# Optimization experiments

Measured on AMD Instinct MI355X. Metric: run time of the kernel, lower is better.

The kernel has to match this reference:

```python
import jax, jax.numpy as jnp
import numpy as np

B, N, F = 32, 64, 128   # batch, nodes, input features (F == hidden_dim)
E = N * (N - 1)         # fully-connected directed edges = 4032
H, D = 4, 64            # heads, out_dim per head
ALPHA = 0.2             # leaky relu slope


def setup_inputs() -> dict:
    key = jax.random.key(0)
    ks = jax.random.split(key, 16)
    v_self = jax.random.normal(ks[0], (B, N, F), dtype=jnp.float32)
    # fully-connected one-hot sender/receiver matrices [E, N], broadcast to [B, E, N]
    pairs = np.array([(i, j) for i in range(N) for j in range(N) if i != j])
    send = np.zeros((E, N), np.float32); send[np.arange(E), pairs[:, 0]] = 1.0
    rec = np.zeros((E, N), np.float32); rec[np.arange(E), pairs[:, 1]] = 1.0
    rel_send = jnp.broadcast_to(jnp.asarray(send), (B, E, N))
    rel_rec = jnp.broadcast_to(jnp.asarray(rec), (B, E, N))
    s = 0.05
    return {
        "v_self": v_self,
        "rel_rec": rel_rec,
        "rel_send": rel_send,
        "W_proj": jax.random.normal(ks[1], (H * D, F), dtype=jnp.float32) * s,
        "a_fwd": jax.random.normal(ks[2], (H, D), dtype=jnp.float32) * s,
        "a_bwd": jax.random.normal(ks[3], (H, D), dtype=jnp.float32) * s,
        "We1": jax.random.normal(ks[4], (D, 2 * D), dtype=jnp.float32) * s,
        "be1": jnp.zeros((D,), jnp.float32),
        "We2": jax.random.normal(ks[5], (D, D), dtype=jnp.float32) * s,
        "be2": jnp.zeros((D,), jnp.float32),
        "Wv1": jax.random.normal(ks[6], (F, D), dtype=jnp.float32) * s,
        "bv1": jnp.zeros((F,), jnp.float32),
        "Wv2": jax.random.normal(ks[7], (F, F), dtype=jnp.float32) * s,
        "bv2": jnp.zeros((F,), jnp.float32),
        "Wv3": jax.random.normal(ks[8], (D, F), dtype=jnp.float32) * s,
        "bv3": jnp.zeros((D,), jnp.float32),
    }


def _leaky(x):
    return jnp.where(x >= 0, x, ALPHA * x)


def reference(v_self, rel_rec, rel_send, W_proj, a_fwd, a_bwd,
              We1, be1, We2, be2, Wv1, bv1, Wv2, bv2, Wv3, bv3):
    # project: [B,N,F] -> [B,N,H,D]
    v_proj = (v_self @ W_proj.T).reshape(B, N, H, D)
    # gather to edges via one-hot adjacency (v_src==h_src, v_tgt==h_tgt in original)
    h_src = jnp.einsum('ben,bnhd->behd', rel_send, v_proj)
    h_tgt = jnp.einsum('ben,bnhd->behd', rel_rec, v_proj)
    attn_ij = _leaky(jnp.einsum('behd,hd->beh', h_src, a_fwd)) / 500.0
    attn_ji = _leaky(jnp.einsum('behd,hd->beh', h_tgt, a_bwd)) / 500.0
    attn_max = jnp.maximum(attn_ij, attn_ji)
    # NOTE: original applies exp twice (exp of exp); reproduced faithfully
    e_ij = jnp.exp(jnp.exp(attn_ij - attn_max))
    e_ji = jnp.exp(jnp.exp(attn_ji - attn_max))
    alpha_sum = e_ij + e_ji
    alpha_ij = e_ij / alpha_sum   # [B,E,H]
    alpha_ji = e_ji / alpha_sum
    edge_input = jnp.concatenate(
        [alpha_ij[..., None] * h_src, alpha_ji[..., None] * h_tgt], axis=-1)  # [B,E,H,2D]
    # f_CG_e: Linear(2D->D), ReLU, Linear(D->D) on last dim
    e_cg = jax.nn.relu(edge_input @ We1.T + be1) @ We2.T + be2
    edge_weighted = e_cg * alpha_ij[..., None]                               # [B,E,H,D]
    # scatter back to nodes
    v_social = jnp.einsum('behd,ben->bnhd', edge_weighted, rel_rec)          # [B,N,H,D]
    # f_CG_v: Linear(D->F), ReLU, Linear(F->F), ReLU, Linear(F->D)
    x = jax.nn.relu(v_social @ Wv1.T + bv1)
    x = jax.nn.relu(x @ Wv2.T + bv2)
    x = x @ Wv3.T + bv3
    v_out = x.reshape(B, N, H * D)  # concat_heads=True
    return (v_out, alpha_ij)
```

## Files before the change

kernel.cpp:

```cpp
#include <hip/hip_runtime.h>

#define B_ 32
#define N_ 64
#define F_ 128
#define E_ 4032
#define H_ 4
#define D_ 64

typedef __bf16 bf16x8 __attribute__((ext_vector_type(8)));
typedef __bf16 bf16x4 __attribute__((ext_vector_type(4)));
typedef float  f32x4  __attribute__((ext_vector_type(4)));


__global__ __launch_bounds__(256) void k_proj(
    const float* __restrict__ v_self, const float* __restrict__ W_proj,
    const float* __restrict__ We1,
    const float* __restrict__ a_fwd, const float* __restrict__ a_bwd,
    float* __restrict__ s_fwd, float* __restrict__ s_bwd,
    __bf16* __restrict__ u_src, __bf16* __restrict__ u_tgt)
{
    const int t = threadIdx.x;
    const int w = t >> 6, l = t & 63;
    const int q = l >> 4, lr = l & 15;
    const int node0 = blockIdx.x * 8;

    __shared__ __bf16 Av[16 * 136];
    __shared__ __bf16 P_lds[8 * 288];

    {
        int row = t >> 5, c0 = (t & 31) * 4;
        float4 v = *(const float4*)(v_self + (size_t)(node0 + row) * 128 + c0);
        bf16x4 bv; bv[0]=(__bf16)v.x; bv[1]=(__bf16)v.y; bv[2]=(__bf16)v.z; bv[3]=(__bf16)v.w;
        *(bf16x4*)&Av[row * 136 + c0] = bv;
        bf16x4 z = {};
        *(bf16x4*)&Av[(row + 8) * 136 + c0] = z;
    }
    __syncthreads();

    f32x4 acc[4] = {};
#pragma unroll
    for (int ks = 0; ks < 4; ++ks) {
        bf16x8 a = *(const bf16x8*)&Av[lr * 136 + ks * 32 + q * 8];
#pragma unroll
        for (int ct = 0; ct < 4; ++ct) {
            const float4* wr = (const float4*)(W_proj + (size_t)(w * 64 + ct * 16 + lr) * 128 + ks * 32 + q * 8);
            float4 w0 = wr[0], w1 = wr[1];
            bf16x8 b;
            b[0]=(__bf16)w0.x; b[1]=(__bf16)w0.y; b[2]=(__bf16)w0.z; b[3]=(__bf16)w0.w;
            b[4]=(__bf16)w1.x; b[5]=(__bf16)w1.y; b[6]=(__bf16)w1.z; b[7]=(__bf16)w1.w;
            acc[ct] = __builtin_amdgcn_mfma_f32_16x16x32_bf16(a, b, acc[ct], 0, 0, 0);
        }
    }

    {
        float pf[4] = {0,0,0,0}, pb[4] = {0,0,0,0};
#pragma unroll
        for (int ct = 0; ct < 4; ++ct) {
            float af = a_fwd[w * 64 + ct * 16 + lr];
            float ab = a_bwd[w * 64 + ct * 16 + lr];
#pragma unroll
            for (int r = 0; r < 4; ++r) { pf[r] += acc[ct][r] * af; pb[r] += acc[ct][r] * ab; }
        }
#pragma unroll
        for (int m = 1; m < 16; m <<= 1) {
#pragma unroll
            for (int r = 0; r < 4; ++r) { pf[r] += __shfl_xor(pf[r], m); pb[r] += __shfl_xor(pb[r], m); }
        }
        if (lr == 0 && q < 2) {
#pragma unroll
            for (int r = 0; r < 4; ++r) {
                int node = q * 4 + r;
                float x = pf[r]; x = (x >= 0.f ? x : 0.2f * x) * 0.002f;
                float y = pb[r]; y = (y >= 0.f ? y : 0.2f * y) * 0.002f;
                s_fwd[(node0 + node) * 4 + w] = x;
                s_bwd[(node0 + node) * 4 + w] = y;
            }
        }
    }
    if (q < 2) {
#pragma unroll
        for (int ct = 0; ct < 4; ++ct)
#pragma unroll
            for (int r = 0; r < 4; ++r)
                P_lds[(q * 4 + r) * 288 + w * 72 + ct * 16 + lr] = (__bf16)acc[ct][r];
    }
    __syncthreads();

    const int rt = w & 1, mm = w >> 1;
    const int rr = rt * 16 + lr, an = rr >> 2, ah = rr & 3;
    f32x4 uacc[4] = {};
#pragma unroll
    for (int ks = 0; ks < 2; ++ks) {
        bf16x8 a = *(const bf16x8*)&P_lds[an * 288 + ah * 72 + ks * 32 + q * 8];
#pragma unroll
        for (int ct = 0; ct < 4; ++ct) {
            const float4* wr = (const float4*)(We1 + (size_t)(ct * 16 + lr) * 128 + mm * 64 + ks * 32 + q * 8);
            float4 w0 = wr[0], w1 = wr[1];
            bf16x8 b;
            b[0]=(__bf16)w0.x; b[1]=(__bf16)w0.y; b[2]=(__bf16)w0.z; b[3]=(__bf16)w0.w;
            b[4]=(__bf16)w1.x; b[5]=(__bf16)w1.y; b[6]=(__bf16)w1.z; b[7]=(__bf16)w1.w;
            uacc[ct] = __builtin_amdgcn_mfma_f32_16x16x32_bf16(a, b, uacc[ct], 0, 0, 0);
        }
    }
    __bf16* up = (mm == 0) ? u_src : u_tgt;
#pragma unroll
    for (int ct = 0; ct < 4; ++ct)
#pragma unroll
        for (int r = 0; r < 4; ++r) {
            int row = rt * 16 + q * 4 + r;
            up[(size_t)(node0 * 4 + row) * 64 + ct * 16 + lr] = (__bf16)uacc[ct][r];
        }
}

__global__ __launch_bounds__(256) void k_edge(
    const float* __restrict__ s_fwd, const float* __restrict__ s_bwd,
    const __bf16* __restrict__ u_src, const __bf16* __restrict__ u_tgt,
    const float* __restrict__ be1,
    const float* __restrict__ Wv1, const float* __restrict__ We2,
    const float* __restrict__ be2, const float* __restrict__ Wv2,
    const float* __restrict__ Wv3,
    __bf16* __restrict__ g_out, float* __restrict__ suma_out,
    float* __restrict__ out_alpha,
    __bf16* __restrict__ M1bf, float* __restrict__ wb,
    __bf16* __restrict__ Wv2bf, __bf16* __restrict__ Wv3bf)
{
    const int t = threadIdx.x;
    const int blk = blockIdx.x;

    if (blk >= B_ * N_) {
        const int pid = (blk - B_ * N_) * 256 + t;
        const int f = pid >> 6, k = pid & 63;
        float acc = 0.f;
        for (int d = 0; d < 64; ++d)
            acc += Wv1[f * 64 + d] * We2[d * 64 + k];
        M1bf[pid] = (__bf16)acc;
        float p = Wv1[f * 64 + k] * be2[k];
#pragma unroll
        for (int m = 1; m < 64; m <<= 1) p += __shfl_xor(p, m);
        if (k == 0) wb[f] = p;
        Wv2bf[pid]        = (__bf16)Wv2[pid];
        Wv2bf[pid + 8192] = (__bf16)Wv2[pid + 8192];
        Wv3bf[pid]        = (__bf16)Wv3[pid];
        return;
    }

    const int h = t >> 6, d = t & 63;
    const int b = blk >> 6, x = blk & 63;
    const int j = x;

    __shared__ float aij_s[4][64];

    if (t < 252) {
        const int jj = t >> 2, h2 = t & 3;
        const int j2 = jj + (jj >= x ? 1 : 0);
        float sfi = s_fwd[(b * 64 + x) * 4 + h2];
        float sbj = s_bwd[(b * 64 + j2) * 4 + h2];
        float m = fmaxf(sfi, sbj);
        float eij = __expf(__expf(sfi - m));
        float eji = __expf(__expf(sbj - m));
        out_alpha[((size_t)b * E_ + x * 63 + jj) * 4 + h2] = eij / (eij + eji);
    }

    {
        const int i = d;
        float sfi = s_fwd[(b * 64 + i) * 4 + h];
        float sbj = s_bwd[(b * 64 + j) * 4 + h];
        float m = fmaxf(sfi, sbj);
        float eij = __expf(__expf(sfi - m));
        float eji = __expf(__expf(sbj - m));
        float aij = eij / (eij + eji);
        if (i == j) aij = 0.f;
        aij_s[h][i] = aij;
        float sa = aij;
#pragma unroll
        for (int m2 = 1; m2 < 64; m2 <<= 1) sa += __shfl_xor(sa, m2);
        if (i == 0) suma_out[(b * 64 + j) * 4 + h] = sa;
    }
    __syncthreads();

    const float utv = (float)u_tgt[((size_t)(b * 64 + j) * 4 + h) * 64 + d];
    const float ub  = utv + be1[d];
    const __bf16* usp = u_src + ((size_t)(b * 64) * 4 + h) * 64 + d;
    float g = 0.f;
#pragma unroll 8
    for (int i = 0; i < 64; ++i) {
        float a = aij_s[h][i];
        float usv = (float)usp[(size_t)i * 256];
        float hp = fmaf(a, usv - utv, ub);
        g = fmaf(a, fmaxf(hp, 0.f), g);
    }
    g_out[((size_t)(b * 64 + j) * 4 + h) * 64 + d] = (__bf16)g;
}

__global__ __launch_bounds__(256) void k_mlp(
    const __bf16* __restrict__ g_bf, const float* __restrict__ suma_in,
    const __bf16* __restrict__ M1bf, const float* __restrict__ wb,
    const float* __restrict__ bv1,
    const __bf16* __restrict__ Wv2bf, const float* __restrict__ bv2,
    const __bf16* __restrict__ Wv3bf, const float* __restrict__ bv3,
    float* __restrict__ v_out)
{
    const int t = threadIdx.x;
    const int w = t >> 6, l = t & 63;
    const int q = l >> 4, lr = l & 15;
    const int rows0 = blockIdx.x * 32;

    __shared__ __bf16 X1[32 * 136];
    __shared__ __bf16 X2[32 * 136];

    const int rt = w & 1, ch = w >> 1;

    f32x4 acc1[4] = {};
#pragma unroll
    for (int ks = 0; ks < 2; ++ks) {
        bf16x8 a = *(const bf16x8*)(g_bf + (size_t)(rows0 + rt * 16 + lr) * 64 + ks * 32 + q * 8);
#pragma unroll
        for (int ct = 0; ct < 4; ++ct) {
            bf16x8 b = *(const bf16x8*)(M1bf + (size_t)(ch * 64 + ct * 16 + lr) * 64 + ks * 32 + q * 8);
            acc1[ct] = __builtin_amdgcn_mfma_f32_16x16x32_bf16(a, b, acc1[ct], 0, 0, 0);
        }
    }
    float sml[4];
#pragma unroll
    for (int r = 0; r < 4; ++r) sml[r] = suma_in[rows0 + rt * 16 + q * 4 + r];
#pragma unroll
    for (int ct = 0; ct < 4; ++ct) {
        int f = ch * 64 + ct * 16 + lr;
        float wbf = wb[f], b1 = bv1[f];
#pragma unroll
        for (int r = 0; r < 4; ++r) {
            float xv = acc1[ct][r] + sml[r] * wbf + b1;
            X1[(rt * 16 + q * 4 + r) * 136 + f] = (__bf16)fmaxf(xv, 0.f);
        }
    }
    __syncthreads();

    f32x4 acc2[4] = {};
#pragma unroll
    for (int ks = 0; ks < 4; ++ks) {
        bf16x8 a = *(const bf16x8*)&X1[(rt * 16 + lr) * 136 + ks * 32 + q * 8];
#pragma unroll
        for (int ct = 0; ct < 4; ++ct) {
            bf16x8 b = *(const bf16x8*)(Wv2bf + (size_t)(ch * 64 + ct * 16 + lr) * 128 + ks * 32 + q * 8);
            acc2[ct] = __builtin_amdgcn_mfma_f32_16x16x32_bf16(a, b, acc2[ct], 0, 0, 0);
        }
    }
#pragma unroll
    for (int ct = 0; ct < 4; ++ct) {
        int f = ch * 64 + ct * 16 + lr;
        float b2 = bv2[f];
#pragma unroll
        for (int r = 0; r < 4; ++r) {
            float xv = acc2[ct][r] + b2;
            X2[(rt * 16 + q * 4 + r) * 136 + f] = (__bf16)fmaxf(xv, 0.f);
        }
    }
    __syncthreads();

    f32x4 acc3[2] = {};
#pragma unroll
    for (int ks = 0; ks < 4; ++ks) {
        bf16x8 a = *(const bf16x8*)&X2[(rt * 16 + lr) * 136 + ks * 32 + q * 8];
#pragma unroll
        for (int ct = 0; ct < 2; ++ct) {
            bf16x8 b = *(const bf16x8*)(Wv3bf + (size_t)(ch * 32 + ct * 16 + lr) * 128 + ks * 32 + q * 8);
            acc3[ct] = __builtin_amdgcn_mfma_f32_16x16x32_bf16(a, b, acc3[ct], 0, 0, 0);
        }
    }
#pragma unroll
    for (int ct = 0; ct < 2; ++ct) {
        int dd = ch * 32 + ct * 16 + lr;
        float b3 = bv3[dd];
#pragma unroll
        for (int r = 0; r < 4; ++r)
            v_out[(size_t)(rows0 + rt * 16 + q * 4 + r) * 64 + dd] = acc3[ct][r] + b3;
    }
}

extern "C" void kernel_launch(void* const* d_in, const int* in_sizes, int n_in,
                              void* d_out, int out_size, void* d_ws, size_t ws_size,
                              hipStream_t stream) {
    (void)in_sizes; (void)n_in; (void)out_size; (void)ws_size;
    const float* v_self = (const float*)d_in[0];
    const float* W_proj = (const float*)d_in[3];
    const float* a_fwd  = (const float*)d_in[4];
    const float* a_bwd  = (const float*)d_in[5];
    const float* We1    = (const float*)d_in[6];
    const float* be1    = (const float*)d_in[7];
    const float* We2    = (const float*)d_in[8];
    const float* be2    = (const float*)d_in[9];
    const float* Wv1    = (const float*)d_in[10];
    const float* bv1    = (const float*)d_in[11];
    const float* Wv2    = (const float*)d_in[12];
    const float* bv2    = (const float*)d_in[13];
    const float* Wv3    = (const float*)d_in[14];
    const float* bv3    = (const float*)d_in[15];

    float* ws = (float*)d_ws;
    float*  s_fwd = ws;
    float*  s_bwd = ws + 8192;
    float*  suma  = ws + 16384;
    float*  wb    = ws + 24576;
    __bf16* M1bf  = (__bf16*)(ws + 24704);
    __bf16* Wv2bf = (__bf16*)(ws + 28800);
    __bf16* Wv3bf = (__bf16*)(ws + 36992);
    __bf16* u_src = (__bf16*)(ws + 61568);
    __bf16* u_tgt = (__bf16*)(ws + 323712);
    __bf16* g_bf  = (__bf16*)(ws + 585856);

    float* v_out = (float*)d_out;
    float* alpha = v_out + (size_t)B_ * N_ * H_ * D_;

    hipLaunchKernelGGL(k_proj, dim3(B_ * N_ / 8), dim3(256), 0, stream,
                       v_self, W_proj, We1, a_fwd, a_bwd, s_fwd, s_bwd, u_src, u_tgt);
    hipLaunchKernelGGL(k_edge, dim3(B_ * N_ + 32), dim3(256), 0, stream,
                       s_fwd, s_bwd, u_src, u_tgt, be1, Wv1, We2, be2, Wv2, Wv3,
                       g_bf, suma, alpha, M1bf, wb, Wv2bf, Wv3bf);
    hipLaunchKernelGGL(k_mlp, dim3(B_ * N_ * H_ / 32), dim3(256), 0, stream,
                       g_bf, suma, M1bf, wb, bv1, Wv2bf, bv2, Wv3bf, bv3, v_out);
}
```

Baseline: 29.76 us.

## Fuse edge aggregation and node MLP into one kernel, move weight prep into projection

Merges the edge-aggregation kernel and the node MLP kernel into one launch. Each block now handles 8 target nodes of one batch: it stages the batch's u_src in LDS as fp32 and keeps g and suma in LDS instead of writing them to global memory. The weight-precompute blocks move into the projection kernel, so the whole op takes two launches instead of three. In exchange, the grid shrinks from about 2k blocks to 256, and the 64KB+ LDS footprint per block lowers occupancy.

Result: slower. 31.43 us (+5.6%).

```diff
diff --git a/kernel.cpp b/kernel.cpp
--- a/kernel.cpp
+++ b/kernel.cpp
@@ -16,10 +16,33 @@
     const float* __restrict__ v_self, const float* __restrict__ W_proj,
     const float* __restrict__ We1,
     const float* __restrict__ a_fwd, const float* __restrict__ a_bwd,
+    const float* __restrict__ Wv1, const float* __restrict__ We2,
+    const float* __restrict__ be2, const float* __restrict__ Wv2,
+    const float* __restrict__ Wv3,
     float* __restrict__ s_fwd, float* __restrict__ s_bwd,
-    __bf16* __restrict__ u_src, __bf16* __restrict__ u_tgt)
+    __bf16* __restrict__ u_src, __bf16* __restrict__ u_tgt,
+    __bf16* __restrict__ M1bf, float* __restrict__ wb,
+    __bf16* __restrict__ Wv2bf, __bf16* __restrict__ Wv3bf)
 {
     const int t = threadIdx.x;
+
+    if (blockIdx.x >= B_ * N_ / 8) {
+        const int pid = (blockIdx.x - B_ * N_ / 8) * 256 + t;
+        const int f = pid >> 6, k = pid & 63;
+        float acc = 0.f;
+        for (int dd = 0; dd < 64; ++dd)
+            acc += Wv1[f * 64 + dd] * We2[dd * 64 + k];
+        M1bf[pid] = (__bf16)acc;
+        float p = Wv1[f * 64 + k] * be2[k];
+#pragma unroll
+        for (int m = 1; m < 64; m <<= 1) p += __shfl_xor(p, m);
+        if (k == 0) wb[f] = p;
+        Wv2bf[pid]        = (__bf16)Wv2[pid];
+        Wv2bf[pid + 8192] = (__bf16)Wv2[pid + 8192];
+        Wv3bf[pid]        = (__bf16)Wv3[pid];
+        return;
+    }
+
     const int w = t >> 6, l = t & 63;
     const int q = l >> 4, lr = l & 15;
     const int node0 = blockIdx.x * 8;
@@ -112,117 +135,135 @@
         }
 }
 
-__global__ __launch_bounds__(256) void k_edge(
+__global__ __launch_bounds__(256) void k_fused(
     const float* __restrict__ s_fwd, const float* __restrict__ s_bwd,
     const __bf16* __restrict__ u_src, const __bf16* __restrict__ u_tgt,
     const float* __restrict__ be1,
-    const float* __restrict__ Wv1, const float* __restrict__ We2,
-    const float* __restrict__ be2, const float* __restrict__ Wv2,
-    const float* __restrict__ Wv3,
-    __bf16* __restrict__ g_out, float* __restrict__ suma_out,
-    float* __restrict__ out_alpha,
-    __bf16* __restrict__ M1bf, float* __restrict__ wb,
-    __bf16* __restrict__ Wv2bf, __bf16* __restrict__ Wv3bf)
-{
-    const int t = threadIdx.x;
-    const int blk = blockIdx.x;
-
-    if (blk >= B_ * N_) {
-        const int pid = (blk - B_ * N_) * 256 + t;
-        const int f = pid >> 6, k = pid & 63;
-        float acc = 0.f;
-        for (int d = 0; d < 64; ++d)
-            acc += Wv1[f * 64 + d] * We2[d * 64 + k];
-        M1bf[pid] = (__bf16)acc;
-        float p = Wv1[f * 64 + k] * be2[k];
-#pragma unroll
-        for (int m = 1; m < 64; m <<= 1) p += __shfl_xor(p, m);
-        if (k == 0) wb[f] = p;
-        Wv2bf[pid]        = (__bf16)Wv2[pid];
-        Wv2bf[pid + 8192] = (__bf16)Wv2[pid + 8192];
-        Wv3bf[pid]        = (__bf16)Wv3[pid];
-        return;
-    }
-
-    const int h = t >> 6, d = t & 63;
-    const int b = blk >> 6, x = blk & 63;
-    const int j = x;
-
-    __shared__ float aij_s[4][64];
-
-    if (t < 252) {
-        const int jj = t >> 2, h2 = t & 3;
-        const int j2 = jj + (jj >= x ? 1 : 0);
-        float sfi = s_fwd[(b * 64 + x) * 4 + h2];
-        float sbj = s_bwd[(b * 64 + j2) * 4 + h2];
-        float m = fmaxf(sfi, sbj);
-        float eij = __expf(__expf(sfi - m));
-        float eji = __expf(__expf(sbj - m));
-        out_alpha[((size_t)b * E_ + x * 63 + jj) * 4 + h2] = eij / (eij + eji);
-    }
-
-    {
-        const int i = d;
-        float sfi = s_fwd[(b * 64 + i) * 4 + h];
-        float sbj = s_bwd[(b * 64 + j) * 4 + h];
-        float m = fmaxf(sfi, sbj);
-        float eij = __expf(__expf(sfi - m));
-        float eji = __expf(__expf(sbj - m));
-        float aij = eij / (eij + eji);
-        if (i == j) aij = 0.f;
-        aij_s[h][i] = aij;
-        float sa = aij;
-#pragma unroll
-        for (int m2 = 1; m2 < 64; m2 <<= 1) sa += __shfl_xor(sa, m2);
-        if (i == 0) suma_out[(b * 64 + j) * 4 + h] = sa;
-    }
-    __syncthreads();
-
-    const float utv = (float)u_tgt[((size_t)(b * 64 + j) * 4 + h) * 64 + d];
-    const float ub  = utv + be1[d];
-    const __bf16* usp = u_src + ((size_t)(b * 64) * 4 + h) * 64 + d;
-    float g = 0.f;
-#pragma unroll 8
-    for (int i = 0; i < 64; ++i) {
-        float a = aij_s[h][i];
-        float usv = (float)usp[(size_t)i * 256];
-        float hp = fmaf(a, usv - utv, ub);
-        g = fmaf(a, fmaxf(hp, 0.f), g);
-    }
-    g_out[((size_t)(b * 64 + j) * 4 + h) * 64 + d] = (__bf16)g;
-}
-
-__global__ __launch_bounds__(256) void k_mlp(
-    const __bf16* __restrict__ g_bf, const float* __restrict__ suma_in,
     const __bf16* __restrict__ M1bf, const float* __restrict__ wb,
     const float* __restrict__ bv1,
     const __bf16* __restrict__ Wv2bf, const float* __restrict__ bv2,
     const __bf16* __restrict__ Wv3bf, const float* __restrict__ bv3,
-    float* __restrict__ v_out)
+    float* __restrict__ v_out, float* __restrict__ out_alpha)
 {
     const int t = threadIdx.x;
-    const int w = t >> 6, l = t & 63;
+    const int h = t >> 6, d = t & 63;
+    const int b = blockIdx.x >> 3, oct = blockIdx.x & 7;
+    const int j0 = oct * 8;
+
+    __shared__ float u_l[4][64][64];
+    __shared__ float ut_l[8][4][64];
+    __shared__ float aij_l[4][64][8];
+    __shared__ float suma_l[32];
+    __shared__ __bf16 g_l[32 * 72];
+
+    {
+        const __bf16* ub = u_src + (size_t)b * 16384;
+        for (int idx = t * 8; idx < 16384; idx += 256 * 8) {
+            bf16x8 v = *(const bf16x8*)(ub + idx);
+            int i = idx >> 8, col = idx & 255;
+            float* dst = &u_l[col >> 6][i][col & 63];
+#pragma unroll
+            for (int z = 0; z < 8; ++z) dst[z] = (float)v[z];
+        }
+        const __bf16* utp = u_tgt + ((size_t)(b * 64 + j0)) * 256;
+        {
+            int idx = t * 8;
+            bf16x8 v = *(const bf16x8*)(utp + idx);
+            int j = idx >> 8, col = idx & 255;
+            float* dst = &ut_l[j][col >> 6][col & 63];
+#pragma unroll
+            for (int z = 0; z < 8; ++z) dst[z] = (float)v[z];
+        }
+    }
+
+    {
+        const int i = d;
+        float sfi = s_fwd[(b * 64 + i) * 4 + h];
+        float areg[8];
+#pragma unroll
+        for (int j = 0; j < 8; ++j) {
+            float sbj = s_bwd[(b * 64 + j0 + j) * 4 + h];
+            float m = fmaxf(sfi, sbj);
+            float eij = __expf(__expf(sfi - m));
+            float eji = __expf(__expf(sbj - m));
+            float aij = eij / (eij + eji);
+            if (i == j0 + j) aij = 0.f;
+            areg[j] = aij;
+        }
+        f32x4 a0 = {areg[0], areg[1], areg[2], areg[3]};
+        f32x4 a1 = {areg[4], areg[5], areg[6], areg[7]};
+        *(f32x4*)&aij_l[h][i][0] = a0;
+        *(f32x4*)&aij_l[h][i][4] = a1;
+#pragma unroll
+        for (int j = 0; j < 8; ++j) {
+            float sa = areg[j];
+#pragma unroll
+            for (int m2 = 1; m2 < 64; m2 <<= 1) sa += __shfl_xor(sa, m2);
+            if (i == 0) suma_l[j * 4 + h] = sa;
+        }
+    }
+    if (t < 252) {
+        const int jj = t >> 2, h2 = t & 3;
+#pragma unroll
+        for (int s = 0; s < 8; ++s) {
+            int i2 = j0 + s;
+            int j2 = jj + (jj >= i2 ? 1 : 0);
+            float sfi = s_fwd[(b * 64 + i2) * 4 + h2];
+            float sbj = s_bwd[(b * 64 + j2) * 4 + h2];
+            float m = fmaxf(sfi, sbj);
+            float eij = __expf(__expf(sfi - m));
+            float eji = __expf(__expf(sbj - m));
+            out_alpha[((size_t)b * E_ + i2 * 63 + jj) * 4 + h2] = eij / (eij + eji);
+        }
+    }
+    __syncthreads();
+
+    {
+        const float be1d = be1[d];
+        float utv[8], utb[8];
+#pragma unroll
+        for (int j = 0; j < 8; ++j) { utv[j] = ut_l[j][h][d]; utb[j] = utv[j] + be1d; }
+        float gacc[8] = {};
+        for (int i = 0; i < 64; ++i) {
+            float usv = u_l[h][i][d];
+            f32x4 a0 = *(const f32x4*)&aij_l[h][i][0];
+            f32x4 a1 = *(const f32x4*)&aij_l[h][i][4];
+#pragma unroll
+            for (int j = 0; j < 4; ++j) {
+                float a = a0[j];
+                float hp = fmaf(a, usv - utv[j], utb[j]);
+                gacc[j] = fmaf(a, fmaxf(hp, 0.f), gacc[j]);
+                float a2 = a1[j];
+                float hp2 = fmaf(a2, usv - utv[4 + j], utb[4 + j]);
+                gacc[4 + j] = fmaf(a2, fmaxf(hp2, 0.f), gacc[4 + j]);
+            }
+        }
+#pragma unroll
+        for (int j = 0; j < 8; ++j)
+            g_l[(j * 4 + h) * 72 + d] = (__bf16)gacc[j];
+    }
+    __syncthreads();
+
+    __bf16* X1 = (__bf16*)&u_l[0][0][0];
+    __bf16* X2 = X1 + 32 * 136;
+    const int w = h, l = t & 63;
     const int q = l >> 4, lr = l & 15;
-    const int rows0 = blockIdx.x * 32;
-
-    __shared__ __bf16 X1[32 * 136];
-    __shared__ __bf16 X2[32 * 136];
-
     const int rt = w & 1, ch = w >> 1;
+    const int rows_base = (b * 64 + j0) * 4;
 
     f32x4 acc1[4] = {};
 #pragma unroll
     for (int ks = 0; ks < 2; ++ks) {
-        bf16x8 a = *(const bf16x8*)(g_bf + (size_t)(rows0 + rt * 16 + lr) * 64 + ks * 32 + q * 8);
-#pragma unroll
-        for (int ct = 0; ct < 4; ++ct) {
-            bf16x8 b = *(const bf16x8*)(M1bf + (size_t)(ch * 64 + ct * 16 + lr) * 64 + ks * 32 + q * 8);
-            acc1[ct] = __builtin_amdgcn_mfma_f32_16x16x32_bf16(a, b, acc1[ct], 0, 0, 0);
+        bf16x8 a = *(const bf16x8*)&g_l[(rt * 16 + lr) * 72 + ks * 32 + q * 8];
+#pragma unroll
+        for (int ct = 0; ct < 4; ++ct) {
+            bf16x8 bfr = *(const bf16x8*)(M1bf + (size_t)(ch * 64 + ct * 16 + lr) * 64 + ks * 32 + q * 8);
+            acc1[ct] = __builtin_amdgcn_mfma_f32_16x16x32_bf16(a, bfr, acc1[ct], 0, 0, 0);
         }
     }
     float sml[4];
 #pragma unroll
-    for (int r = 0; r < 4; ++r) sml[r] = suma_in[rows0 + rt * 16 + q * 4 + r];
+    for (int r = 0; r < 4; ++r) sml[r] = suma_l[rt * 16 + q * 4 + r];
 #pragma unroll
     for (int ct = 0; ct < 4; ++ct) {
         int f = ch * 64 + ct * 16 + lr;
@@ -241,8 +282,8 @@
         bf16x8 a = *(const bf16x8*)&X1[(rt * 16 + lr) * 136 + ks * 32 + q * 8];
 #pragma unroll
         for (int ct = 0; ct < 4; ++ct) {
-            bf16x8 b = *(const bf16x8*)(Wv2bf + (size_t)(ch * 64 + ct * 16 + lr) * 128 + ks * 32 + q * 8);
-            acc2[ct] = __builtin_amdgcn_mfma_f32_16x16x32_bf16(a, b, acc2[ct], 0, 0, 0);
+            bf16x8 bfr = *(const bf16x8*)(Wv2bf + (size_t)(ch * 64 + ct * 16 + lr) * 128 + ks * 32 + q * 8);
+            acc2[ct] = __builtin_amdgcn_mfma_f32_16x16x32_bf16(a, bfr, acc2[ct], 0, 0, 0);
         }
     }
 #pragma unroll
@@ -263,8 +304,8 @@
         bf16x8 a = *(const bf16x8*)&X2[(rt * 16 + lr) * 136 + ks * 32 + q * 8];
 #pragma unroll
         for (int ct = 0; ct < 2; ++ct) {
-            bf16x8 b = *(const bf16x8*)(Wv3bf + (size_t)(ch * 32 + ct * 16 + lr) * 128 + ks * 32 + q * 8);
-            acc3[ct] = __builtin_amdgcn_mfma_f32_16x16x32_bf16(a, b, acc3[ct], 0, 0, 0);
+            bf16x8 bfr = *(const bf16x8*)(Wv3bf + (size_t)(ch * 32 + ct * 16 + lr) * 128 + ks * 32 + q * 8);
+            acc3[ct] = __builtin_amdgcn_mfma_f32_16x16x32_bf16(a, bfr, acc3[ct], 0, 0, 0);
         }
     }
 #pragma unroll
@@ -273,7 +314,7 @@
         float b3 = bv3[dd];
 #pragma unroll
         for (int r = 0; r < 4; ++r)
-            v_out[(size_t)(rows0 + rt * 16 + q * 4 + r) * 64 + dd] = acc3[ct][r] + b3;
+            v_out[(size_t)(rows_base + rt * 16 + q * 4 + r) * 64 + dd] = acc3[ct][r] + b3;
     }
 }
 
@@ -299,23 +340,20 @@
     float* ws = (float*)d_ws;
     float*  s_fwd = ws;
     float*  s_bwd = ws + 8192;
-    float*  suma  = ws + 16384;
     float*  wb    = ws + 24576;
     __bf16* M1bf  = (__bf16*)(ws + 24704);
     __bf16* Wv2bf = (__bf16*)(ws + 28800);
     __bf16* Wv3bf = (__bf16*)(ws + 36992);
     __bf16* u_src = (__bf16*)(ws + 61568);
     __bf16* u_tgt = (__bf16*)(ws + 323712);
-    __bf16* g_bf  = (__bf16*)(ws + 585856);
 
     float* v_out = (float*)d_out;
     float* alpha = v_out + (size_t)B_ * N_ * H_ * D_;
 
-    hipLaunchKernelGGL(k_proj, dim3(B_ * N_ / 8), dim3(256), 0, stream,
-                       v_self, W_proj, We1, a_fwd, a_bwd, s_fwd, s_bwd, u_src, u_tgt);
-    hipLaunchKernelGGL(k_edge, dim3(B_ * N_ + 32), dim3(256), 0, stream,
-                       s_fwd, s_bwd, u_src, u_tgt, be1, Wv1, We2, be2, Wv2, Wv3,
-                       g_bf, suma, alpha, M1bf, wb, Wv2bf, Wv3bf);
-    hipLaunchKernelGGL(k_mlp, dim3(B_ * N_ * H_ / 32), dim3(256), 0, stream,
-                       g_bf, suma, M1bf, wb, bv1, Wv2bf, bv2, Wv3bf, bv3, v_out);
+    hipLaunchKernelGGL(k_proj, dim3(B_ * N_ / 8 + 32), dim3(256), 0, stream,
+                       v_self, W_proj, We1, a_fwd, a_bwd, Wv1, We2, be2, Wv2, Wv3,
+                       s_fwd, s_bwd, u_src, u_tgt, M1bf, wb, Wv2bf, Wv3bf);
+    hipLaunchKernelGGL(k_fused, dim3(B_ * N_ / 8), dim3(256), 0, stream,
+                       s_fwd, s_bwd, u_src, u_tgt, be1, M1bf, wb, bv1,
+                       Wv2bf, bv2, Wv3bf, bv3, v_out, alpha);
 }
```
